# Performance work log

Hardware: AMD Instinct MI355X
Metric: run time of the kernel (lower is better)

Reference implementation:

```python
import jax, jax.numpy as jnp
import numpy as np

N_NODES = 50000
N_EDGES = 800000
N_INC = 64
E_OUTC = 64
HS1 = 128
HS2 = 128
LN_EPS = 1e-5


def setup_inputs() -> dict:
    key = jax.random.key(0)
    ks = jax.random.split(key, 8)
    scale1 = 1.0 / np.sqrt(N_INC + E_OUTC)
    scale2 = 1.0 / np.sqrt(HS1)
    return {
        "x": jax.random.normal(ks[0], (N_NODES, N_INC), dtype=jnp.float32),
        "edge_attr": jax.random.normal(ks[1], (N_EDGES, E_OUTC), dtype=jnp.float32),
        "edge_index": jax.random.randint(ks[2], (2, N_EDGES), 0, N_NODES, dtype=jnp.int64)
        if jax.config.jax_enable_x64 else jax.random.randint(ks[2], (2, N_EDGES), 0, N_NODES, dtype=jnp.int32),
        "W1": jax.random.normal(ks[3], (N_INC + E_OUTC, HS1), dtype=jnp.float32) * scale1,
        "b1": jnp.zeros((HS1,), dtype=jnp.float32),
        "ln_g": jnp.ones((HS1,), dtype=jnp.float32),
        "ln_b": jnp.zeros((HS1,), dtype=jnp.float32),
        "W2": jax.random.normal(ks[4], (HS1, HS2), dtype=jnp.float32) * scale2,
        "b2": jnp.zeros((HS2,), dtype=jnp.float32),
    }


def reference(x, edge_attr, edge_index, W1, b1, ln_g, ln_b, W2, b2):
    # _agg: gather source nodes, concat with edge features -> [E, n_inc+e_outc]
    row, col = edge_index[0], edge_index[1]
    h = jnp.concatenate([x[row], edge_attr], axis=1)
    # node_mlp_1: Linear -> LayerNorm -> ReLU -> Linear
    h = h @ W1 + b1
    mu = jnp.mean(h, axis=-1, keepdims=True)
    var = jnp.mean(jnp.square(h - mu), axis=-1, keepdims=True)
    h = (h - mu) * jax.lax.rsqrt(var + LN_EPS) * ln_g + ln_b
    h = jax.nn.relu(h)
    h = h @ W2 + b2  # [E, HS2]
    # scatter_mean into destination nodes, dim_size = N
    n = x.shape[0]
    sums = jax.ops.segment_sum(h, col, num_segments=n)
    cnt = jax.ops.segment_sum(jnp.ones((h.shape[0],), dtype=h.dtype), col, num_segments=n)
    return sums / jnp.maximum(cnt, 1.0)[:, None]
```

## Files before the change

kernel.cpp:

```cpp
#include <hip/hip_runtime.h>
#include <hip/hip_bf16.h>


typedef __bf16 bf16x8 __attribute__((ext_vector_type(8)));
typedef float f32x4 __attribute__((ext_vector_type(4)));

#define LN_EPS 1e-5f

__device__ __forceinline__ unsigned short bfbits(float f) {
  return __builtin_bit_cast(unsigned short, (__bf16)f);
}
__device__ __forceinline__ float bflo(unsigned int u) { return __uint_as_float(u << 16); }
__device__ __forceinline__ float bfhi(unsigned int u) { return __uint_as_float(u & 0xffff0000u); }
__device__ __forceinline__ unsigned int pkbf(float a, float b) {
  return (unsigned int)bfbits(a) | ((unsigned int)bfbits(b) << 16);
}

__global__ void hist_kernel(const int* __restrict__ eidx, int* __restrict__ cnt, int E) {
  int e = blockIdx.x * blockDim.x + threadIdx.x;
  if (e < E) atomicAdd(&cnt[eidx[E + e]], 1);
}

__global__ void scan_kernel(const int* __restrict__ cnt, int* __restrict__ off, int n) {
  __shared__ int wsum[16];
  __shared__ int carry_s;
  const int tid = threadIdx.x;
  const int wv = tid >> 6;
  const int ln = tid & 63;
  if (tid == 0) carry_s = 0;
  __syncthreads();
  for (int base = 0; base < n; base += 4096) {
    int i0 = base + tid * 4;
    int a = (i0 < n) ? cnt[i0] : 0;
    int b = (i0 + 1 < n) ? cnt[i0 + 1] : 0;
    int c = (i0 + 2 < n) ? cnt[i0 + 2] : 0;
    int d = (i0 + 3 < n) ? cnt[i0 + 3] : 0;
    int lsum = a + b + c + d;
    int sc = lsum;
#pragma unroll
    for (int dl = 1; dl < 64; dl <<= 1) {
      int t = __shfl_up(sc, dl);
      if (ln >= dl) sc += t;
    }
    if (ln == 63) wsum[wv] = sc;
    __syncthreads();
    int woff = 0;
#pragma unroll
    for (int w = 0; w < 16; ++w) {
      int t = wsum[w];
      if (w < wv) woff += t;
    }
    int excl = carry_s + woff + sc - lsum;
    if (i0 < n) off[i0] = excl;
    if (i0 + 1 < n) off[i0 + 1] = excl + a;
    if (i0 + 2 < n) off[i0 + 2] = excl + a + b;
    if (i0 + 3 < n) off[i0 + 3] = excl + a + b + c;
    __syncthreads();
    if (tid == 1023) carry_s = carry_s + woff + sc;
    __syncthreads();
  }
}

__global__ void scatter_kernel(const int* __restrict__ eidx, const int* __restrict__ off,
                               int* __restrict__ cur, int* __restrict__ perm,
                               int* __restrict__ rowp, int E) {
  int e = blockIdx.x * blockDim.x + threadIdx.x;
  if (e < E) {
    int c = eidx[E + e];
    int p = atomicAdd(&cur[c], 1);
    int pos = off[c] + p;
    perm[pos] = e;
    rowp[pos] = eidx[e];
  }
}

template <bool ATOMIC>
__global__ __launch_bounds__(512, 2) void mlp_kernel(
    const float* __restrict__ x, const float* __restrict__ ea,
    const int* __restrict__ eidx, const int* __restrict__ perm,
    const int* __restrict__ rowp, const int* __restrict__ cnt,
    const float* __restrict__ W1, const float* __restrict__ b1,
    const float* __restrict__ lng, const float* __restrict__ lnb,
    const float* __restrict__ W2, const float* __restrict__ b2,
    float* __restrict__ out, int E, int ntiles) {
  __shared__ __align__(16) unsigned int w1L[2048 * 4];
  __shared__ __align__(16) unsigned int w2L[2048 * 4];
  __shared__ float b1L[128];
  __shared__ float b2L[128];
  __shared__ unsigned int glcL[128];
  __shared__ __align__(16) char hbuf[8][16 * 272];

  const int tid = threadIdx.x;
  const int lane = tid & 63;
  const int wv = tid >> 6;
  const int e15 = lane & 15;
  const int q = lane >> 4;
  char* hb = hbuf[wv];

  for (int c = tid; c < 2048; c += 512) {
    const int fragid = c >> 6;
    const int l = c & 63;
    const int ks = fragid >> 3, mt = fragid & 7;
    const int qq = l >> 4, ee = l & 15;
    const size_t base = (size_t)(ks * 32 + qq * 8) * 128 + mt * 16 + ee;
    unsigned int p1[4], p2[4];
#pragma unroll
    for (int jj = 0; jj < 4; ++jj) {
      p1[jj] = pkbf(W1[base + (size_t)(2 * jj) * 128], W1[base + (size_t)(2 * jj + 1) * 128]);
      p2[jj] = pkbf(W2[base + (size_t)(2 * jj) * 128], W2[base + (size_t)(2 * jj + 1) * 128]);
    }
    uint4 v1 = {p1[0], p1[1], p1[2], p1[3]};
    uint4 v2 = {p2[0], p2[1], p2[2], p2[3]};
    *(uint4*)&w1L[c * 4] = v1;
    *(uint4*)&w2L[c * 4] = v2;
  }
  if (tid < 128) {
    b1L[tid] = b1[tid];
    b2L[tid] = b2[tid];
    glcL[tid] = pkbf(lng[tid], lnb[tid]);
  }
  __syncthreads();

  const int nwav = (gridDim.x * blockDim.x) >> 6;
  const int wid = (blockIdx.x * blockDim.x + tid) >> 6;

  auto mlp_core = [&](const float4 (&raw)[8], f32x4 (&c2)[8]) {
    bf16x8 bfr[4];
#pragma unroll
    for (int ks = 0; ks < 4; ++ks) {
      const float* p0 = (const float*)&raw[2 * ks];
      const float* p1 = (const float*)&raw[2 * ks + 1];
#pragma unroll
      for (int j = 0; j < 4; ++j) {
        bfr[ks][j] = (__bf16)p0[j];
        bfr[ks][4 + j] = (__bf16)p1[j];
      }
    }
    f32x4 c1[8];
#pragma unroll
    for (int mt = 0; mt < 8; ++mt) {
      float4 bv = *(const float4*)&b1L[mt * 16 + q * 4];
      c1[mt][0] = bv.x;
      c1[mt][1] = bv.y;
      c1[mt][2] = bv.z;
      c1[mt][3] = bv.w;
    }
#pragma unroll
    for (int ks = 0; ks < 4; ++ks)
#pragma unroll
      for (int mt = 0; mt < 8; ++mt) {
        bf16x8 wf = __builtin_bit_cast(
            bf16x8, *(const uint4*)&w1L[((ks * 8 + mt) * 64 + lane) * 4]);
        c1[mt] = __builtin_amdgcn_mfma_f32_16x16x32_bf16(wf, bfr[ks], c1[mt], 0, 0, 0);
      }

    float s = 0.f, ss = 0.f;
#pragma unroll
    for (int mt = 0; mt < 8; ++mt)
#pragma unroll
      for (int r = 0; r < 4; ++r) {
        float v = c1[mt][r];
        s += v;
        ss += v * v;
      }
    s += __shfl_xor(s, 16);
    s += __shfl_xor(s, 32);
    ss += __shfl_xor(ss, 16);
    ss += __shfl_xor(ss, 32);
    const float mu = s * 0.0078125f;
    const float var = ss * 0.0078125f - mu * mu;
    const float inv = rsqrtf(var + LN_EPS);
#pragma unroll
    for (int mt = 0; mt < 8; ++mt) {
      uint4 gv = *(const uint4*)&glcL[mt * 16 + q * 4];
      unsigned int g[4] = {gv.x, gv.y, gv.z, gv.w};
      unsigned short u[4];
#pragma unroll
      for (int r = 0; r < 4; ++r) {
        float v = (c1[mt][r] - mu) * inv;
        v = v * bflo(g[r]) + bfhi(g[r]);
        v = fmaxf(v, 0.f);
        u[r] = bfbits(v);
      }
      uint2 w;
      w.x = (unsigned int)u[0] | ((unsigned int)u[1] << 16);
      w.y = (unsigned int)u[2] | ((unsigned int)u[3] << 16);
      *(uint2*)(hb + e15 * 272 + mt * 32 + q * 8) = w;
    }
    bf16x8 hf[4];
#pragma unroll
    for (int ks = 0; ks < 4; ++ks)
      hf[ks] = __builtin_bit_cast(bf16x8, *(const uint4*)(hb + e15 * 272 + ks * 64 + q * 16));
#pragma unroll
    for (int mt = 0; mt < 8; ++mt) {
      float4 bv = *(const float4*)&b2L[mt * 16 + q * 4];
      c2[mt][0] = bv.x;
      c2[mt][1] = bv.y;
      c2[mt][2] = bv.z;
      c2[mt][3] = bv.w;
    }
#pragma unroll
    for (int ks = 0; ks < 4; ++ks)
#pragma unroll
      for (int mt = 0; mt < 8; ++mt) {
        bf16x8 wf = __builtin_bit_cast(
            bf16x8, *(const uint4*)&w2L[((ks * 8 + mt) * 64 + lane) * 4]);
        c2[mt] = __builtin_amdgcn_mfma_f32_16x16x32_bf16(wf, hf[ks], c2[mt], 0, 0, 0);
      }
  };

  auto reduce_store = [&](const f32x4 (&c2)[8], int nd, float inv) {
#pragma unroll
    for (int mt = 0; mt < 8; ++mt) {
      unsigned short u[4];
#pragma unroll
      for (int r = 0; r < 4; ++r) u[r] = bfbits(c2[mt][r]);
      uint2 w;
      w.x = (unsigned int)u[0] | ((unsigned int)u[1] << 16);
      w.y = (unsigned int)u[2] | ((unsigned int)u[3] << 16);
      *(uint2*)(hb + e15 * 272 + mt * 32 + q * 8) = w;
    }
    float acc0 = 0.f, acc1 = 0.f;
    int curn = __shfl(nd, 0);
    float cinv = __shfl(inv, 0);
#pragma unroll
    for (int i = 0; i < 16; ++i) {
      int ni = __shfl(nd, i);
      float ii = __shfl(inv, i);
      if (ni != curn) {
        unsafeAtomicAdd(out + (size_t)curn * 128 + lane * 2, acc0 * cinv);
        unsafeAtomicAdd(out + (size_t)curn * 128 + lane * 2 + 1, acc1 * cinv);
        acc0 = 0.f;
        acc1 = 0.f;
        curn = ni;
        cinv = ii;
      }
      unsigned int v = *(const unsigned int*)(hb + i * 272 + lane * 4);
      acc0 += bflo(v);
      acc1 += bfhi(v);
    }
    unsafeAtomicAdd(out + (size_t)curn * 128 + lane * 2, acc0 * cinv);
    unsafeAtomicAdd(out + (size_t)curn * 128 + lane * 2 + 1, acc1 * cinv);
  };

#define LOADRAW(dst, rowv, ev)                              \
  do {                                                      \
    const float* xr_ = x + (size_t)(rowv)*64;               \
    const float* ar_ = ea + (size_t)(ev)*64;                \
    dst[0] = *(const float4*)(xr_ + q * 8);                 \
    dst[1] = *(const float4*)(xr_ + q * 8 + 4);             \
    dst[2] = *(const float4*)(xr_ + 32 + q * 8);            \
    dst[3] = *(const float4*)(xr_ + 32 + q * 8 + 4);        \
    dst[4] = *(const float4*)(ar_ + q * 8);                 \
    dst[5] = *(const float4*)(ar_ + q * 8 + 4);             \
    dst[6] = *(const float4*)(ar_ + 32 + q * 8);            \
    dst[7] = *(const float4*)(ar_ + 32 + q * 8 + 4);        \
  } while (0)

  if constexpr (!ATOMIC) {
    int tA = wid;
    if (tA >= ntiles) return;
    int pA = tA * 16 + e15;
    int eA = perm[pA];
    int rowA = rowp[pA];
    int ndA = eidx[E + eA];
    float invA = 1.f / (float)cnt[ndA];
    int tB = tA + nwav;
    int tBc = (tB < ntiles) ? tB : tA;
    int pB = tBc * 16 + e15;
    int eB = perm[pB];
    int rowB = rowp[pB];
    int ndB = eidx[E + eB];
    float invB = 1.f / (float)cnt[ndB];
    float4 rawA[8], rawB[8];
    LOADRAW(rawA, rowA, eA);

    for (int tb = tA; tb < ntiles; tb += 2 * nwav) {
      {
        int tn = tb + 2 * nwav;
        int tc = (tn < ntiles) ? tn : tb;
        int pn = tc * 16 + e15;
        int eAn = perm[pn];
        int rAn = rowp[pn];
        int nAn = eidx[E + eAn];
        float iAn = 1.f / (float)cnt[nAn];
        LOADRAW(rawB, rowB, eB);
        f32x4 c2[8];
        mlp_core(rawA, c2);
        reduce_store(c2, ndA, invA);
        eA = eAn;
        rowA = rAn;
        ndA = nAn;
        invA = iAn;
      }
      {
        int tcur = tb + nwav;
        int tn = tb + 3 * nwav;
        int tc = (tn < ntiles) ? tn : tb;
        int pn = tc * 16 + e15;
        int eBn = perm[pn];
        int rBn = rowp[pn];
        int nBn = eidx[E + eBn];
        float iBn = 1.f / (float)cnt[nBn];
        LOADRAW(rawA, rowA, eA);
        if (tcur < ntiles) {
          f32x4 c2[8];
          mlp_core(rawB, c2);
          reduce_store(c2, ndB, invB);
        }
        eB = eBn;
        rowB = rBn;
        ndB = nBn;
        invB = iBn;
      }
    }
  } else {
    for (int t = wid; t < ntiles; t += nwav) {
      const int pos = t * 16 + e15;
      const int e = pos;
      const int row = eidx[e];
      const int cl = eidx[E + e];
      float4 raw[8];
      LOADRAW(raw, row, e);
      f32x4 c2[8];
      mlp_core(raw, c2);
      float* op = out + (size_t)cl * 128 + q * 4;
#pragma unroll
      for (int mt = 0; mt < 8; ++mt)
#pragma unroll
        for (int r = 0; r < 4; ++r) unsafeAtomicAdd(op + mt * 16 + r, c2[mt][r]);
    }
  }
#undef LOADRAW
}

__global__ void divide_kernel(float* __restrict__ out, const int* __restrict__ cnt, int N) {
  int i = blockIdx.x * blockDim.x + threadIdx.x;
  if (i >= N * 32) return;
  int node = i >> 5;
  float s = 1.f / (float)(cnt[node] > 0 ? cnt[node] : 1);
  float4* p = (float4*)out + i;
  float4 v = *p;
  v.x *= s;
  v.y *= s;
  v.z *= s;
  v.w *= s;
  *p = v;
}

extern "C" void kernel_launch(void* const* d_in, const int* in_sizes, int n_in,
                              void* d_out, int out_size, void* d_ws, size_t ws_size,
                              hipStream_t stream) {
  const float* x = (const float*)d_in[0];
  const float* ea = (const float*)d_in[1];
  const int* eidx = (const int*)d_in[2];
  const float* W1 = (const float*)d_in[3];
  const float* b1 = (const float*)d_in[4];
  const float* lng = (const float*)d_in[5];
  const float* lnb = (const float*)d_in[6];
  const float* W2 = (const float*)d_in[7];
  const float* b2 = (const float*)d_in[8];
  float* out = (float*)d_out;

  const int N = in_sizes[0] / 64;
  const int E = in_sizes[1] / 64;
  const int ntiles = E / 16;
  const size_t permB = (size_t)E * 4;
  const size_t cB = (size_t)N * 4;
  const size_t need = 2 * permB + 3 * cB;
  const int eblocks = (E + 255) / 256;

  if (ws_size >= need) {
    int* perm = (int*)d_ws;
    int* rowp = perm + E;
    int* cnt = rowp + E;
    int* cur = cnt + N;
    int* off = cur + N;
    hipMemsetAsync(out, 0, (size_t)out_size * 4, stream);
    hipMemsetAsync(cnt, 0, 2 * cB, stream);
    hist_kernel<<<eblocks, 256, 0, stream>>>(eidx, cnt, E);
    scan_kernel<<<1, 1024, 0, stream>>>(cnt, off, N);
    scatter_kernel<<<eblocks, 256, 0, stream>>>(eidx, off, cur, perm, rowp, E);
    mlp_kernel<false><<<256, 512, 0, stream>>>(x, ea, eidx, perm, rowp, cnt, W1, b1,
                                               lng, lnb, W2, b2, out, E, ntiles);
  } else {
    int* cnt = (int*)d_ws;
    hipMemsetAsync(out, 0, (size_t)out_size * 4, stream);
    hipMemsetAsync(cnt, 0, cB, stream);
    hist_kernel<<<eblocks, 256, 0, stream>>>(eidx, cnt, E);
    mlp_kernel<true><<<256, 512, 0, stream>>>(x, ea, eidx, nullptr, nullptr, cnt, W1,
                                              b1, lng, lnb, W2, b2, out, E, ntiles);
    divide_kernel<<<(N * 32 + 255) / 256, 256, 0, stream>>>(out, cnt, N);
  }
}
```

Baseline: 489.2 us.

## Fuse histogram, scan and scatter into persistent MLP kernel with grid barriers

Merges the histogram, prefix-scan and CSR scatter passes into the MLP kernel. The kernel now launches one block per CU and separates the phases with a software grid barrier built on device-scope atomics. The goal is to drop three kernel launches and the single-block serial scan, replacing the scan with a parallel two-level block scan. The cost is grid-barrier spin overhead and a risk of deadlock if all blocks are not co-resident. Grid size drops from 256 to the CU count, which changes the occupancy of the MLP phase.

```diff
diff --git a/kernel.cpp b/kernel.cpp
--- a/kernel.cpp
+++ b/kernel.cpp
@@ -16,83 +16,60 @@
   return (unsigned int)bfbits(a) | ((unsigned int)bfbits(b) << 16);
 }
 
+__device__ __forceinline__ void gbar(int* slot) {
+  __syncthreads();
+  if (threadIdx.x == 0) {
+    __threadfence();
+    __hip_atomic_fetch_add(slot, 1, __ATOMIC_ACQ_REL, __HIP_MEMORY_SCOPE_AGENT);
+    while (__hip_atomic_load(slot, __ATOMIC_ACQUIRE, __HIP_MEMORY_SCOPE_AGENT) <
+           (int)gridDim.x)
+      __builtin_amdgcn_s_sleep(2);
+  }
+  __syncthreads();
+}
+
 __global__ void hist_kernel(const int* __restrict__ eidx, int* __restrict__ cnt, int E) {
   int e = blockIdx.x * blockDim.x + threadIdx.x;
   if (e < E) atomicAdd(&cnt[eidx[E + e]], 1);
 }
 
-__global__ void scan_kernel(const int* __restrict__ cnt, int* __restrict__ off, int n) {
-  __shared__ int wsum[16];
-  __shared__ int carry_s;
-  const int tid = threadIdx.x;
-  const int wv = tid >> 6;
-  const int ln = tid & 63;
-  if (tid == 0) carry_s = 0;
-  __syncthreads();
-  for (int base = 0; base < n; base += 4096) {
-    int i0 = base + tid * 4;
-    int a = (i0 < n) ? cnt[i0] : 0;
-    int b = (i0 + 1 < n) ? cnt[i0 + 1] : 0;
-    int c = (i0 + 2 < n) ? cnt[i0 + 2] : 0;
-    int d = (i0 + 3 < n) ? cnt[i0 + 3] : 0;
-    int lsum = a + b + c + d;
-    int sc = lsum;
-#pragma unroll
-    for (int dl = 1; dl < 64; dl <<= 1) {
-      int t = __shfl_up(sc, dl);
-      if (ln >= dl) sc += t;
-    }
-    if (ln == 63) wsum[wv] = sc;
-    __syncthreads();
-    int woff = 0;
-#pragma unroll
-    for (int w = 0; w < 16; ++w) {
-      int t = wsum[w];
-      if (w < wv) woff += t;
-    }
-    int excl = carry_s + woff + sc - lsum;
-    if (i0 < n) off[i0] = excl;
-    if (i0 + 1 < n) off[i0 + 1] = excl + a;
-    if (i0 + 2 < n) off[i0 + 2] = excl + a + b;
-    if (i0 + 3 < n) off[i0 + 3] = excl + a + b + c;
-    __syncthreads();
-    if (tid == 1023) carry_s = carry_s + woff + sc;
-    __syncthreads();
-  }
-}
-
-__global__ void scatter_kernel(const int* __restrict__ eidx, const int* __restrict__ off,
-                               int* __restrict__ cur, int* __restrict__ perm,
-                               int* __restrict__ rowp, int E) {
-  int e = blockIdx.x * blockDim.x + threadIdx.x;
-  if (e < E) {
-    int c = eidx[E + e];
-    int p = atomicAdd(&cur[c], 1);
-    int pos = off[c] + p;
-    perm[pos] = e;
-    rowp[pos] = eidx[e];
-  }
-}
-
-template <bool ATOMIC>
+__global__ void divide_kernel(float* __restrict__ out, const int* __restrict__ cnt, int N) {
+  int i = blockIdx.x * blockDim.x + threadIdx.x;
+  if (i >= N * 32) return;
+  int node = i >> 5;
+  float s = 1.f / (float)(cnt[node] > 0 ? cnt[node] : 1);
+  float4* p = (float4*)out + i;
+  float4 v = *p;
+  v.x *= s;
+  v.y *= s;
+  v.z *= s;
+  v.w *= s;
+  *p = v;
+}
+
+template <bool FUSED>
 __global__ __launch_bounds__(512, 2) void mlp_kernel(
     const float* __restrict__ x, const float* __restrict__ ea,
-    const int* __restrict__ eidx, const int* __restrict__ perm,
-    const int* __restrict__ rowp, const int* __restrict__ cnt,
-    const float* __restrict__ W1, const float* __restrict__ b1,
-    const float* __restrict__ lng, const float* __restrict__ lnb,
-    const float* __restrict__ W2, const float* __restrict__ b2,
-    float* __restrict__ out, int E, int ntiles) {
+    const int* __restrict__ eidx, int* __restrict__ perm,
+    int* __restrict__ rowp, int* __restrict__ cnt, int* __restrict__ cur,
+    int* __restrict__ off, int* __restrict__ blkSum, int* __restrict__ blkOff,
+    int* __restrict__ bar, const float* __restrict__ W1,
+    const float* __restrict__ b1, const float* __restrict__ lng,
+    const float* __restrict__ lnb, const float* __restrict__ W2,
+    const float* __restrict__ b2, float* __restrict__ out, int N, int E,
+    int ntiles) {
   __shared__ __align__(16) unsigned int w1L[2048 * 4];
   __shared__ __align__(16) unsigned int w2L[2048 * 4];
   __shared__ float b1L[128];
   __shared__ float b2L[128];
   __shared__ unsigned int glcL[128];
   __shared__ __align__(16) char hbuf[8][16 * 272];
+  __shared__ int wsumS[8];
 
   const int tid = threadIdx.x;
   const int lane = tid & 63;
   const int wv = tid >> 6;
+  const int ln = lane;
   const int e15 = lane & 15;
   const int q = lane >> 4;
   char* hb = hbuf[wv];
@@ -119,10 +96,82 @@
     b2L[tid] = b2[tid];
     glcL[tid] = pkbf(lng[tid], lnb[tid]);
   }
-  __syncthreads();
-
-  const int nwav = (gridDim.x * blockDim.x) >> 6;
-  const int wid = (blockIdx.x * blockDim.x + tid) >> 6;
+
+  const int nb = gridDim.x;
+  const int gthreads = nb * 512;
+  const int gtid = blockIdx.x * 512 + tid;
+
+  if constexpr (FUSED) {
+    for (int e = gtid; e < E; e += gthreads) atomicAdd(&cnt[eidx[E + e]], 1);
+    gbar(&bar[0]);
+
+    const int CHUNK = (N + nb - 1) / nb;
+    const int base = blockIdx.x * CHUNK;
+    const int myi = base + tid;
+    int v = 0;
+    if (tid < CHUNK && myi < N) v = cnt[myi];
+    int sc = v;
+#pragma unroll
+    for (int d = 1; d < 64; d <<= 1) {
+      int t = __shfl_up(sc, d);
+      if (ln >= d) sc += t;
+    }
+    if (ln == 63) wsumS[wv] = sc;
+    __syncthreads();
+    int woff = 0;
+#pragma unroll
+    for (int w = 0; w < 8; ++w) {
+      int t = wsumS[w];
+      if (w < wv) woff += t;
+    }
+    const int excl = woff + sc - v;
+    if (tid == 0) {
+      int s = 0;
+#pragma unroll
+      for (int w = 0; w < 8; ++w) s += wsumS[w];
+      blkSum[blockIdx.x] = s;
+    }
+    gbar(&bar[1]);
+
+    if (blockIdx.x == 0) {
+      int v2 = (tid < nb) ? blkSum[tid] : 0;
+      int sc2 = v2;
+#pragma unroll
+      for (int d = 1; d < 64; d <<= 1) {
+        int t = __shfl_up(sc2, d);
+        if (ln >= d) sc2 += t;
+      }
+      __syncthreads();
+      if (ln == 63) wsumS[wv] = sc2;
+      __syncthreads();
+      int woff2 = 0;
+#pragma unroll
+      for (int w = 0; w < 8; ++w) {
+        int t = wsumS[w];
+        if (w < wv) woff2 += t;
+      }
+      if (tid < nb) blkOff[tid] = woff2 + sc2 - v2;
+    }
+    gbar(&bar[2]);
+
+    const int boff = blkOff[blockIdx.x];
+    if (tid < CHUNK && myi < N) off[myi] = excl + boff;
+    gbar(&bar[3]);
+
+    for (int e = gtid; e < E; e += gthreads) {
+      int c = eidx[E + e];
+      int p = atomicAdd(&cur[c], 1);
+      int pos = off[c] + p;
+      perm[pos] = e;
+      rowp[pos] = eidx[e];
+    }
+    gbar(&bar[4]);
+  } else {
+    __syncthreads();
+  }
+
+  const int nwav = gthreads >> 6;
+  const int wid = gtid >> 6;
 
   auto mlp_core = [&](const float4 (&raw)[8], f32x4 (&c2)[8]) {
     bf16x8 bfr[4];
@@ -257,7 +306,7 @@
     dst[7] = *(const float4*)(ar_ + 32 + q * 8 + 4);        \
   } while (0)
 
-  if constexpr (!ATOMIC) {
+  if constexpr (FUSED) {
     int tA = wid;
     if (tA >= ntiles) return;
     int pA = tA * 16 + e15;
@@ -334,20 +383,6 @@
 #undef LOADRAW
 }
 
-__global__ void divide_kernel(float* __restrict__ out, const int* __restrict__ cnt, int N) {
-  int i = blockIdx.x * blockDim.x + threadIdx.x;
-  if (i >= N * 32) return;
-  int node = i >> 5;
-  float s = 1.f / (float)(cnt[node] > 0 ? cnt[node] : 1);
-  float4* p = (float4*)out + i;
-  float4 v = *p;
-  v.x *= s;
-  v.y *= s;
-  v.z *= s;
-  v.w *= s;
-  *p = v;
-}
-
 extern "C" void kernel_launch(void* const* d_in, const int* in_sizes, int n_in,
                               void* d_out, int out_size, void* d_ws, size_t ws_size,
                               hipStream_t stream) {
@@ -367,29 +402,43 @@
   const int ntiles = E / 16;
   const size_t permB = (size_t)E * 4;
   const size_t cB = (size_t)N * 4;
-  const size_t need = 2 * permB + 3 * cB;
-  const int eblocks = (E + 255) / 256;
-
-  if (ws_size >= need) {
+  const size_t tailI = 3 * (size_t)N + 512 + 16;
+  const size_t need = 2 * permB + tailI * 4;
+
+  static int nb_cached = 0;
+  if (nb_cached == 0) {
+    int dev = 0;
+    hipGetDevice(&dev);
+    hipDeviceProp_t prop;
+    hipGetDeviceProperties(&prop, dev);
+    nb_cached = prop.multiProcessorCount < 256 ? prop.multiProcessorCount : 256;
+  }
+  const int nb = nb_cached;
+
+  if (ws_size >= need && nb >= 98 && (size_t)nb * 512 >= (size_t)512) {
     int* perm = (int*)d_ws;
     int* rowp = perm + E;
     int* cnt = rowp + E;
     int* cur = cnt + N;
     int* off = cur + N;
+    int* blkSum = off + N;
+    int* blkOff = blkSum + 256;
+    int* bar = blkOff + 256;
     hipMemsetAsync(out, 0, (size_t)out_size * 4, stream);
-    hipMemsetAsync(cnt, 0, 2 * cB, stream);
-    hist_kernel<<<eblocks, 256, 0, stream>>>(eidx, cnt, E);
-    scan_kernel<<<1, 1024, 0, stream>>>(cnt, off, N);
-    scatter_kernel<<<eblocks, 256, 0, stream>>>(eidx, off, cur, perm, rowp, E);
-    mlp_kernel<false><<<256, 512, 0, stream>>>(x, ea, eidx, perm, rowp, cnt, W1, b1,
-                                               lng, lnb, W2, b2, out, E, ntiles);
+    hipMemsetAsync(cnt, 0, tailI * 4, stream);
+    mlp_kernel<true><<<nb, 512, 0, stream>>>(x, ea, eidx, perm, rowp, cnt, cur, off,
+                                             blkSum, blkOff, bar, W1, b1, lng, lnb,
+                                             W2, b2, out, N, E, ntiles);
   } else {
     int* cnt = (int*)d_ws;
+    const int eblocks = (E + 255) / 256;
     hipMemsetAsync(out, 0, (size_t)out_size * 4, stream);
     hipMemsetAsync(cnt, 0, cB, stream);
     hist_kernel<<<eblocks, 256, 0, stream>>>(eidx, cnt, E);
-    mlp_kernel<true><<<256, 512, 0, stream>>>(x, ea, eidx, nullptr, nullptr, cnt, W1,
-                                              b1, lng, lnb, W2, b2, out, E, ntiles);
+    mlp_kernel<false><<<256, 512, 0, stream>>>(x, ea, eidx, nullptr, nullptr, cnt,
+                                               nullptr, nullptr, nullptr, nullptr,
+                                               nullptr, W1, b1, lng, lnb, W2, b2,
+                                               out, N, E, ntiles);
     divide_kernel<<<(N * 32 + 255) / 256, 256, 0, stream>>>(out, cnt, N);
   }
 }
```

Measured after the change: 586.3 us. 19.8% more time.
